# Optimization experiments

Hardware: AMD Instinct MI355X
Metric: run time of the kernel (lower is better)

## Reference

```python
import jax, jax.numpy as jnp
import numpy as np

TOP_K = 2

def setup_inputs() -> dict:
    key = jax.random.key(0)
    ks = jax.random.split(key, 8)
    B, T, C, E, I, S = 1, 2048, 2048, 8, 1408, 2816
    s = 0.02  # weight scale for numerical stability
    return {
        "x": jax.random.normal(ks[0], (B, T, C), jnp.float32),
        "gate_w": jax.random.normal(ks[1], (E, C), jnp.float32) * s,
        "w1": jax.random.normal(ks[2], (E, I, C), jnp.float32) * s,
        "w3": jax.random.normal(ks[3], (E, I, C), jnp.float32) * s,
        "w2": jax.random.normal(ks[4], (E, C, I), jnp.float32) * s,
        "sw1": jax.random.normal(ks[5], (S, C), jnp.float32) * s,
        "sw3": jax.random.normal(ks[6], (S, C), jnp.float32) * s,
        "sw2": jax.random.normal(ks[7], (C, S), jnp.float32) * s,
    }

def reference(x, gate_w, w1, w3, w2, sw1, sw3, sw2):
    B, T, C = x.shape
    E = gate_w.shape[0]
    xf = x.reshape(-1, C)                      # [N, C]
    N = xf.shape[0]
    # --- routing: top-k of raw logits, softmax over the k selected logits ---
    logits = xf @ gate_w.T                     # [N, E]
    pv, idx = jax.lax.top_k(logits, TOP_K)     # [N, K]
    pv = jax.nn.softmax(pv.astype(jnp.float32), axis=-1).astype(x.dtype)
    # token-expert combine weights (sum of probs per expert, scatter of top-k)
    tew = jnp.zeros((N, E), x.dtype).at[jnp.arange(N)[:, None], idx].add(pv)
    # --- experts (SwiGLU), computed densely over all experts and masked by tew ---
    h = jax.nn.silu(jnp.einsum('nc,eic->nei', xf, w1)) * jnp.einsum('nc,eic->nei', xf, w3)
    eo = jnp.einsum('nei,eci->nec', h, w2)     # [N, E, C]
    y = jnp.einsum('nec,ne->nc', eo, tew).reshape(B, T, C)
    # --- shared expert on the residual input ---
    sh = (jax.nn.silu(x @ sw1.T) * (x @ sw3.T)) @ sw2.T
    return y + sh
```

## Files before the change

### kernel.cpp

```cpp
#include <hip/hip_runtime.h>

#define DEVI __device__ __forceinline__

typedef __attribute__((ext_vector_type(4))) float f32x4;
typedef __attribute__((ext_vector_type(8))) short bf16x8;

static constexpr int NT = 2048;
static constexpr int CD = 2048;
static constexpr int NE = 8;
static constexpr int ID = 1408;
static constexpr int SD = 2816;
static constexpr int ROWS = 2 * NT;
static constexpr int ROWS_PAD = ROWS + 256;

DEVI unsigned short f2bf(float f) {
  unsigned u = __builtin_bit_cast(unsigned, f);
  u += 0x7fff + ((u >> 16) & 1);
  return (unsigned short)(u >> 16);
}
DEVI float bf2f(unsigned short s) { return __builtin_bit_cast(float, (unsigned)s << 16); }
DEVI float silu_f(float z) { return z / (1.f + __expf(-z)); }

DEVI void gll16(const void* g, void* l) {
  __builtin_amdgcn_global_load_lds((__attribute__((address_space(1))) void*)(void*)g,
                                   (__attribute__((address_space(3))) void*)l, 16, 0, 0);
}

DEVI void bar_sched() {
  __builtin_amdgcn_s_barrier();
  __builtin_amdgcn_sched_barrier(0);
}
DEVI void wait_vm8() { asm volatile("s_waitcnt vmcnt(8)" ::: "memory"); }
DEVI void wait_vm0() { asm volatile("s_waitcnt vmcnt(0)" ::: "memory"); }
DEVI void wait_lgk0() { asm volatile("s_waitcnt lgkmcnt(0)" ::: "memory"); }

DEVI int swz8(int bid, int nwg) {
  constexpr int CH = 8, G = 64;
  int nfull = nwg - (nwg % G);
  if (bid >= nfull) return bid;
  int c = bid / G, r = bid % G;
  return c * G + (r % 8) * CH + (r / 8);
}

__global__ __launch_bounds__(256) void k_cvt(const float* __restrict__ s,
                                             unsigned short* __restrict__ d, int n8)
{
  int i = blockIdx.x * 256 + threadIdx.x;
  int stride = gridDim.x * 256;
  for (; i < n8; i += stride) {
    float4 a = ((const float4*)s)[2 * i];
    float4 b = ((const float4*)s)[2 * i + 1];
    ushort4 p0 = make_ushort4(f2bf(a.x), f2bf(a.y), f2bf(a.z), f2bf(a.w));
    ushort4 p1 = make_ushort4(f2bf(b.x), f2bf(b.y), f2bf(b.z), f2bf(b.w));
    ((ushort4*)d)[2 * i]     = p0;
    ((ushort4*)d)[2 * i + 1] = p1;
  }
}

__global__ __launch_bounds__(64) void k_router(const float* __restrict__ x,
    const float* __restrict__ gw, int* __restrict__ counts,
    int* __restrict__ eidx, int* __restrict__ posn, float* __restrict__ probs)
{
  const int n = blockIdx.x;
  const int lane = threadIdx.x;
  const float4* xr = (const float4*)(x + (size_t)n * CD);
  float acc[NE];
#pragma unroll
  for (int e = 0; e < NE; ++e) acc[e] = 0.f;
  for (int i = lane; i < CD / 4; i += 64) {
    float4 xv = xr[i];
#pragma unroll
    for (int e = 0; e < NE; ++e) {
      float4 gv = ((const float4*)(gw + (size_t)e * CD))[i];
      acc[e] += xv.x * gv.x + xv.y * gv.y + xv.z * gv.z + xv.w * gv.w;
    }
  }
#pragma unroll
  for (int e = 0; e < NE; ++e) {
    float v = acc[e];
#pragma unroll
    for (int off = 32; off > 0; off >>= 1) v += __shfl_down(v, off);
    acc[e] = v;
  }
  if (lane == 0) {
    int b0 = 0; float m0 = acc[0];
#pragma unroll
    for (int e = 1; e < NE; ++e) if (acc[e] > m0) { m0 = acc[e]; b0 = e; }
    int b1 = -1; float m1 = 0.f;
#pragma unroll
    for (int e = 0; e < NE; ++e) {
      if (e == b0) continue;
      if (b1 < 0 || acc[e] > m1) { m1 = acc[e]; b1 = e; }
    }
    float d = __expf(m1 - m0);
    float inv = 1.f / (1.f + d);
    eidx[2 * n] = b0; eidx[2 * n + 1] = b1;
    probs[2 * n] = inv; probs[2 * n + 1] = d * inv;
    posn[2 * n] = atomicAdd(&counts[b0], 1);
    posn[2 * n + 1] = atomicAdd(&counts[b1], 1);
  }
}

__global__ void k_scan(const int* __restrict__ counts, int* __restrict__ bases) {
  if (threadIdx.x == 0) {
    int s = 0;
    for (int e = 0; e < NE; ++e) { bases[e] = s; s += counts[e]; }
  }
}

__global__ __launch_bounds__(256) void k_build(const int* __restrict__ eidx,
    const int* __restrict__ posn, const int* __restrict__ bases,
    int* __restrict__ rows_of, int* __restrict__ row2tok)
{
  int n = blockIdx.x * 256 + threadIdx.x;
  if (n >= NT) return;
#pragma unroll
  for (int k = 0; k < 2; ++k) {
    int e = eidx[2 * n + k];
    int row = bases[e] + posn[2 * n + k];
    rows_of[2 * n + k] = row;
    row2tok[row] = n;
  }
}

__global__ __launch_bounds__(512, 2) void k_up(
    const unsigned short* __restrict__ xb,
    const unsigned short* __restrict__ w1b, const unsigned short* __restrict__ w3b,
    const unsigned short* __restrict__ sw1b, const unsigned short* __restrict__ sw3b,
    unsigned short* __restrict__ h, unsigned short* __restrict__ hs,
    const int* __restrict__ counts, const int* __restrict__ bases,
    const int* __restrict__ row2tok)
{
  extern __shared__ char sm[];
  constexpr int NSH = (NT / 256) * (SD / 128);
  constexpr int NWG = NSH + NE * (ID / 128) * (NT / 256);
  constexpr int NSTEP = CD / 64;

  int lin = swz8((int)blockIdx.x, NWG);
  int cls, mx, pn, e = 0;
  if (lin < NSH) { cls = 0; mx = lin % 8; pn = lin / 8; }
  else { cls = 1; int r = lin - NSH; mx = r % 8; r /= 8; pn = r % 11; e = r / 11; }

  int M = NT, baserow = 0;
  if (cls) { M = counts[e]; if (mx * 256 >= M) return; baserow = bases[e]; }
  const int m0 = mx * 256, n0 = pn * 128;

  const unsigned short* B1 = cls ? w1b + ((size_t)e * ID + n0) * CD : sw1b + (size_t)n0 * CD;
  const unsigned short* B3 = cls ? w3b + ((size_t)e * ID + n0) * CD : sw3b + (size_t)n0 * CD;

  const int tid = threadIdx.x, l = tid & 63, w = tid >> 6;
  const int wr = w >> 2, wn = w & 3;
  const int slot = ((tid & 7) ^ ((tid >> 3) & 7)) * 16;

  const char* aP[4];
#pragma unroll
  for (int t = 0; t < 4; ++t) {
    int r = t * 64 + (tid >> 3);
    const unsigned short* rb;
    if (cls) {
      int grow = m0 + r; int gr = grow < M ? grow : 0;
      rb = xb + (size_t)row2tok[baserow + gr] * CD;
    } else {
      rb = xb + (size_t)(m0 + r) * CD;
    }
    aP[t] = (const char*)rb + slot;
  }
  const char* bP1[2]; const char* bP3[2];
#pragma unroll
  for (int t = 0; t < 2; ++t) {
    int r = t * 64 + (tid >> 3);
    bP1[t] = (const char*)(B1 + (size_t)r * CD) + slot;
    bP3[t] = (const char*)(B3 + (size_t)r * CD) + slot;
  }

  f32x4 acc1[8][2], acc3[8][2];
#pragma unroll
  for (int m = 0; m < 8; ++m)
#pragma unroll
    for (int n = 0; n < 2; ++n) {
      acc1[m][n] = {0.f, 0.f, 0.f, 0.f};
      acc3[m][n] = {0.f, 0.f, 0.f, 0.f};
    }

  const int lrow = l & 15, lkg = l >> 4, l7 = l & 7;
  const int ao0 = (lkg ^ l7) * 16, ao1 = ((4 + lkg) ^ l7) * 16;

  auto stageF = [&](char* base, size_t kb) {
    char* sA = base; char* sB1 = base + 32768; char* sB3 = base + 49152;
#pragma unroll
    for (int t = 0; t < 4; ++t) gll16(aP[t] + kb, sA + t * 8192 + tid * 16);
#pragma unroll
    for (int t = 0; t < 2; ++t) {
      gll16(bP1[t] + kb, sB1 + t * 8192 + tid * 16);
      gll16(bP3[t] + kb, sB3 + t * 8192 + tid * 16);
    }
  };
  auto computeF = [&](const char* base) {
    const char* sA = base; const char* sB1 = base + 32768; const char* sB3 = base + 49152;
#pragma unroll
    for (int kk = 0; kk < 2; ++kk) {
      const int ao = kk ? ao1 : ao0;
      bf16x8 af[8];
#pragma unroll
      for (int m = 0; m < 8; ++m)
        af[m] = *(const bf16x8*)(sA + (wr * 128 + m * 16 + lrow) * 128 + ao);
#pragma unroll
      for (int n = 0; n < 2; ++n) {
        bf16x8 b1 = *(const bf16x8*)(sB1 + (wn * 32 + n * 16 + lrow) * 128 + ao);
        bf16x8 b3 = *(const bf16x8*)(sB3 + (wn * 32 + n * 16 + lrow) * 128 + ao);
#pragma unroll
        for (int m = 0; m < 8; ++m) {
          acc1[m][n] = __builtin_amdgcn_mfma_f32_16x16x32_bf16(af[m], b1, acc1[m][n], 0, 0, 0);
          acc3[m][n] = __builtin_amdgcn_mfma_f32_16x16x32_bf16(af[m], b3, acc3[m][n], 0, 0, 0);
        }
      }
    }
  };

  char* s0 = sm; char* s1 = sm + 65536;
  stageF(s0, 0);
  int t = 0;
  for (; t < NSTEP - 2; t += 2) {
    stageF(s1, (size_t)(t + 1) * 128);
    wait_vm8(); bar_sched();
    computeF(s0);
    wait_lgk0(); bar_sched();
    stageF(s0, (size_t)(t + 2) * 128);
    wait_vm8(); bar_sched();
    computeF(s1);
    wait_lgk0(); bar_sched();
  }
  stageF(s1, (size_t)(NSTEP - 1) * 128);
  wait_vm8(); bar_sched();
  computeF(s0);
  wait_vm0(); bar_sched();
  computeF(s1);

#pragma unroll
  for (int m = 0; m < 8; ++m) {
    int rb_ = m0 + wr * 128 + m * 16 + lkg * 4;
#pragma unroll
    for (int j = 0; j < 4; ++j) {
      int grow = rb_ + j;
      if (cls && grow >= M) continue;
#pragma unroll
      for (int n = 0; n < 2; ++n) {
        int gcol = n0 + wn * 32 + n * 16 + lrow;
        float hh = silu_f(acc1[m][n][j]) * acc3[m][n][j];
        if (cls) h[(size_t)(baserow + grow) * ID + gcol] = f2bf(hh);
        else     hs[(size_t)grow * SD + gcol] = f2bf(hh);
      }
    }
  }
}

__global__ __launch_bounds__(512, 2) void k_down(
    const unsigned short* __restrict__ h, const unsigned short* __restrict__ hs,
    const unsigned short* __restrict__ w2b, const unsigned short* __restrict__ sw2b,
    unsigned short* __restrict__ eo, float* __restrict__ y,
    const int* __restrict__ counts, const int* __restrict__ bases)
{
  extern __shared__ char sm[];
  constexpr int NRT = NE * (CD / 256) * (NT / 256);
  constexpr int NWG = NRT + (CD / 256) * (NT / 256);

  int lin = swz8((int)blockIdx.x, NWG);
  int cls, mx, pn, e = 0;
  if (lin < NRT) { cls = 1; mx = lin % 8; int r = lin / 8; pn = r % 8; e = r / 8; }
  else { cls = 0; int r = lin - NRT; mx = r % 8; pn = r / 8; }

  int M = NT, baserow = 0;
  if (cls) { M = counts[e]; if (mx * 256 >= M) return; baserow = bases[e]; }
  const int m0 = mx * 256, n0 = pn * 256;
  const int KD_ = cls ? ID : SD;
  const int nstep = KD_ / 64;

  const unsigned short* B = cls ? w2b + ((size_t)e * CD + n0) * ID : sw2b + (size_t)n0 * SD;

  const int tid = threadIdx.x, l = tid & 63, w = tid >> 6;
  const int wr = w >> 2, wn = w & 3;
  const int slot = ((tid & 7) ^ ((tid >> 3) & 7)) * 16;

  const char* aP[4]; const char* bP[4];
#pragma unroll
  for (int t = 0; t < 4; ++t) {
    int r = t * 64 + (tid >> 3);
    const unsigned short* rb = cls ? h + (size_t)(baserow + m0 + r) * ID
                                   : hs + (size_t)(m0 + r) * SD;
    aP[t] = (const char*)rb + slot;
    bP[t] = (const char*)(B + (size_t)r * KD_) + slot;
  }

  f32x4 acc[8][4];
#pragma unroll
  for (int m = 0; m < 8; ++m)
#pragma unroll
    for (int n = 0; n < 4; ++n) acc[m][n] = {0.f, 0.f, 0.f, 0.f};

  const int lrow = l & 15, lkg = l >> 4, l7 = l & 7;
  const int ao0 = (lkg ^ l7) * 16, ao1 = ((4 + lkg) ^ l7) * 16;

  auto stageF = [&](char* base, size_t kb) {
    char* sA = base; char* sB = base + 32768;
#pragma unroll
    for (int t = 0; t < 4; ++t) {
      gll16(aP[t] + kb, sA + t * 8192 + tid * 16);
      gll16(bP[t] + kb, sB + t * 8192 + tid * 16);
    }
  };
  auto computeF = [&](const char* base) {
    const char* sA = base; const char* sB = base + 32768;
#pragma unroll
    for (int kk = 0; kk < 2; ++kk) {
      const int ao = kk ? ao1 : ao0;
      bf16x8 af[8];
#pragma unroll
      for (int m = 0; m < 8; ++m)
        af[m] = *(const bf16x8*)(sA + (wr * 128 + m * 16 + lrow) * 128 + ao);
#pragma unroll
      for (int n = 0; n < 4; ++n) {
        bf16x8 bv = *(const bf16x8*)(sB + (wn * 64 + n * 16 + lrow) * 128 + ao);
#pragma unroll
        for (int m = 0; m < 8; ++m)
          acc[m][n] = __builtin_amdgcn_mfma_f32_16x16x32_bf16(af[m], bv, acc[m][n], 0, 0, 0);
      }
    }
  };

  char* s0 = sm; char* s1 = sm + 65536;
  stageF(s0, 0);
  int t = 0;
  for (; t < nstep - 2; t += 2) {
    stageF(s1, (size_t)(t + 1) * 128);
    wait_vm8(); bar_sched();
    computeF(s0);
    wait_lgk0(); bar_sched();
    stageF(s0, (size_t)(t + 2) * 128);
    wait_vm8(); bar_sched();
    computeF(s1);
    wait_lgk0(); bar_sched();
  }
  stageF(s1, (size_t)(nstep - 1) * 128);
  wait_vm8(); bar_sched();
  computeF(s0);
  wait_vm0(); bar_sched();
  computeF(s1);

#pragma unroll
  for (int m = 0; m < 8; ++m) {
    int rb_ = m0 + wr * 128 + m * 16 + lkg * 4;
#pragma unroll
    for (int j = 0; j < 4; ++j) {
      int grow = rb_ + j;
      if (cls && grow >= M) continue;
#pragma unroll
      for (int n = 0; n < 4; ++n) {
        int gcol = n0 + wn * 64 + n * 16 + lrow;
        float v = acc[m][n][j];
        if (cls) eo[(size_t)(baserow + grow) * CD + gcol] = f2bf(v);
        else     y[(size_t)grow * CD + gcol] = v;
      }
    }
  }
}

__global__ __launch_bounds__(256) void k_combine(float* __restrict__ y,
    const unsigned short* __restrict__ eo, const int* __restrict__ rows_of,
    const float* __restrict__ probs)
{
  const int n = blockIdx.x;
  const int c = threadIdx.x * 8;
  const int r0 = rows_of[2 * n], r1 = rows_of[2 * n + 1];
  const float p0 = probs[2 * n], p1 = probs[2 * n + 1];
  bf16x8 e0 = *(const bf16x8*)(eo + (size_t)r0 * CD + c);
  bf16x8 e1 = *(const bf16x8*)(eo + (size_t)r1 * CD + c);
  float* yp = y + (size_t)n * CD + c;
  float4 y0 = *(float4*)yp, y1 = *(float4*)(yp + 4);
  y0.x += p0 * bf2f((unsigned short)e0[0]) + p1 * bf2f((unsigned short)e1[0]);
  y0.y += p0 * bf2f((unsigned short)e0[1]) + p1 * bf2f((unsigned short)e1[1]);
  y0.z += p0 * bf2f((unsigned short)e0[2]) + p1 * bf2f((unsigned short)e1[2]);
  y0.w += p0 * bf2f((unsigned short)e0[3]) + p1 * bf2f((unsigned short)e1[3]);
  y1.x += p0 * bf2f((unsigned short)e0[4]) + p1 * bf2f((unsigned short)e1[4]);
  y1.y += p0 * bf2f((unsigned short)e0[5]) + p1 * bf2f((unsigned short)e1[5]);
  y1.z += p0 * bf2f((unsigned short)e0[6]) + p1 * bf2f((unsigned short)e1[6]);
  y1.w += p0 * bf2f((unsigned short)e0[7]) + p1 * bf2f((unsigned short)e1[7]);
  *(float4*)yp = y0; *(float4*)(yp + 4) = y1;
}

extern "C" void kernel_launch(void* const* d_in, const int* in_sizes, int n_in,
                              void* d_out, int out_size, void* d_ws, size_t ws_size,
                              hipStream_t stream)
{
  const float* x   = (const float*)d_in[0];
  const float* gw  = (const float*)d_in[1];
  const float* w1  = (const float*)d_in[2];
  const float* w3  = (const float*)d_in[3];
  const float* w2  = (const float*)d_in[4];
  const float* sw1 = (const float*)d_in[5];
  const float* sw3 = (const float*)d_in[6];
  const float* sw2 = (const float*)d_in[7];
  float* y = (float*)d_out;

  char* p = (char*)d_ws;
  auto alloc = [&](size_t b) { char* r = p; p += (b + 255) & ~(size_t)255; return r; };
  int*   counts  = (int*)alloc(NE * 4);
  int*   bases   = (int*)alloc(NE * 4);
  int*   eidx    = (int*)alloc((size_t)NT * 2 * 4);
  int*   posn    = (int*)alloc((size_t)NT * 2 * 4);
  float* probs   = (float*)alloc((size_t)NT * 2 * 4);
  int*   rows_of = (int*)alloc((size_t)NT * 2 * 4);
  int*   row2tok = (int*)alloc((size_t)ROWS * 4);
  unsigned short* xb   = (unsigned short*)alloc((size_t)NT * CD * 2);
  unsigned short* w1b  = (unsigned short*)alloc((size_t)NE * ID * CD * 2);
  unsigned short* w3b  = (unsigned short*)alloc((size_t)NE * ID * CD * 2);
  unsigned short* w2b  = (unsigned short*)alloc((size_t)NE * CD * ID * 2);
  unsigned short* sw1b = (unsigned short*)alloc((size_t)SD * CD * 2);
  unsigned short* sw3b = (unsigned short*)alloc((size_t)SD * CD * 2);
  unsigned short* sw2b = (unsigned short*)alloc((size_t)CD * SD * 2);
  unsigned short* h    = (unsigned short*)alloc((size_t)ROWS_PAD * ID * 2);
  unsigned short* eo   = (unsigned short*)alloc((size_t)ROWS_PAD * CD * 2);
  unsigned short* hs   = (unsigned short*)alloc((size_t)NT * SD * 2);

  hipFuncSetAttribute((const void*)k_up,   hipFuncAttributeMaxDynamicSharedMemorySize, 131072);
  hipFuncSetAttribute((const void*)k_down, hipFuncAttributeMaxDynamicSharedMemorySize, 131072);

  hipMemsetAsync(counts, 0, NE * 4, stream);

  auto cvt = [&](const float* s, unsigned short* d, size_t n) {
    int n8 = (int)(n / 8);
    int grid = (n8 + 255) / 256; if (grid > 2048) grid = 2048;
    k_cvt<<<grid, 256, 0, stream>>>(s, d, n8);
  };
  cvt(x,   xb,   (size_t)NT * CD);
  cvt(w1,  w1b,  (size_t)NE * ID * CD);
  cvt(w3,  w3b,  (size_t)NE * ID * CD);
  cvt(w2,  w2b,  (size_t)NE * CD * ID);
  cvt(sw1, sw1b, (size_t)SD * CD);
  cvt(sw3, sw3b, (size_t)SD * CD);
  cvt(sw2, sw2b, (size_t)CD * SD);

  k_router<<<NT, 64, 0, stream>>>(x, gw, counts, eidx, posn, probs);
  k_scan<<<1, 64, 0, stream>>>(counts, bases);
  k_build<<<NT / 256, 256, 0, stream>>>(eidx, posn, bases, rows_of, row2tok);

  {
    constexpr int NWG = (NT / 256) * (SD / 128) + NE * (ID / 128) * (NT / 256);
    k_up<<<NWG, 512, 131072, stream>>>(xb, w1b, w3b, sw1b, sw3b, h, hs,
                                       counts, bases, row2tok);
  }
  {
    constexpr int NWG = NE * (CD / 256) * (NT / 256) + (CD / 256) * (NT / 256);
    k_down<<<NWG, 512, 131072, stream>>>(h, hs, w2b, sw2b, eo, y, counts, bases);
  }
  k_combine<<<NT, 256, 0, stream>>>(y, eo, rows_of, probs);
}
```

Measured before the change: 468.9 us.

## Restructure GEMM main loops into ping-pong register-fragment pipeline with split staging

Both GEMM kernels replace the stage-then-compute double-buffer loop with a finer schedule. The LDS-to-register fragment loads for each half of the M tile are interleaved with MFMA batches on the other half. The global-to-LDS loads for the next k-step are split into A and B halves and issued between compute chunks, and s_setprio raises wave priority around the MFMA blocks. The aim is to hide LDS read latency and global load issue behind matrix math, at the cost of one barrier with a full vmcnt(0) wait per k-step and more live fragment registers.

```diff
diff --git a/kernel.cpp b/kernel.cpp
--- a/kernel.cpp
+++ b/kernel.cpp
@@ -30,7 +30,7 @@
   __builtin_amdgcn_s_barrier();
   __builtin_amdgcn_sched_barrier(0);
 }
-DEVI void wait_vm8() { asm volatile("s_waitcnt vmcnt(8)" ::: "memory"); }
+DEVI void sched0() { __builtin_amdgcn_sched_barrier(0); }
 DEVI void wait_vm0() { asm volatile("s_waitcnt vmcnt(0)" ::: "memory"); }
 DEVI void wait_lgk0() { asm volatile("s_waitcnt lgkmcnt(0)" ::: "memory"); }
 
@@ -183,58 +183,71 @@
     }
 
   const int lrow = l & 15, lkg = l >> 4, l7 = l & 7;
-  const int ao0 = (lkg ^ l7) * 16, ao1 = ((4 + lkg) ^ l7) * 16;
-
-  auto stageF = [&](char* base, size_t kb) {
-    char* sA = base; char* sB1 = base + 32768; char* sB3 = base + 49152;
-#pragma unroll
-    for (int t = 0; t < 4; ++t) gll16(aP[t] + kb, sA + t * 8192 + tid * 16);
+
+  auto stage_first = [&](char* base, size_t kb) {
+#pragma unroll
+    for (int t = 0; t < 4; ++t) gll16(aP[t] + kb, base + t * 8192 + tid * 16);
+  };
+  auto stage_second = [&](char* base, size_t kb) {
+    char* sB1 = base + 32768; char* sB3 = base + 49152;
 #pragma unroll
     for (int t = 0; t < 2; ++t) {
       gll16(bP1[t] + kb, sB1 + t * 8192 + tid * 16);
       gll16(bP3[t] + kb, sB3 + t * 8192 + tid * 16);
     }
   };
-  auto computeF = [&](const char* base) {
-    const char* sA = base; const char* sB1 = base + 32768; const char* sB3 = base + 49152;
-#pragma unroll
-    for (int kk = 0; kk < 2; ++kk) {
-      const int ao = kk ? ao1 : ao0;
-      bf16x8 af[8];
-#pragma unroll
-      for (int m = 0; m < 8; ++m)
-        af[m] = *(const bf16x8*)(sA + (wr * 128 + m * 16 + lrow) * 128 + ao);
-#pragma unroll
-      for (int n = 0; n < 2; ++n) {
-        bf16x8 b1 = *(const bf16x8*)(sB1 + (wn * 32 + n * 16 + lrow) * 128 + ao);
-        bf16x8 b3 = *(const bf16x8*)(sB3 + (wn * 32 + n * 16 + lrow) * 128 + ao);
-#pragma unroll
-        for (int m = 0; m < 8; ++m) {
-          acc1[m][n] = __builtin_amdgcn_mfma_f32_16x16x32_bf16(af[m], b1, acc1[m][n], 0, 0, 0);
-          acc3[m][n] = __builtin_amdgcn_mfma_f32_16x16x32_bf16(af[m], b3, acc3[m][n], 0, 0, 0);
-        }
+  auto ldq = [&](bf16x8* fa, bf16x8* fb1, bf16x8* fb3, const char* cur, int mh, int kk) {
+    const char* sA = cur; const char* sB1 = cur + 32768; const char* sB3 = cur + 49152;
+    const int ao = ((kk * 4 + lkg) ^ l7) * 16;
+#pragma unroll
+    for (int m = 0; m < 4; ++m)
+      fa[m] = *(const bf16x8*)(sA + (wr * 128 + mh * 64 + m * 16 + lrow) * 128 + ao);
+#pragma unroll
+    for (int n = 0; n < 2; ++n) {
+      fb1[n] = *(const bf16x8*)(sB1 + (wn * 32 + n * 16 + lrow) * 128 + ao);
+      fb3[n] = *(const bf16x8*)(sB3 + (wn * 32 + n * 16 + lrow) * 128 + ao);
+    }
+  };
+  auto mmq = [&](const bf16x8* fa, const bf16x8* fb1, const bf16x8* fb3, int mh) {
+    __builtin_amdgcn_s_setprio(1);
+#pragma unroll
+    for (int n = 0; n < 2; ++n)
+#pragma unroll
+      for (int m = 0; m < 4; ++m) {
+        acc1[mh * 4 + m][n] = __builtin_amdgcn_mfma_f32_16x16x32_bf16(fa[m], fb1[n], acc1[mh * 4 + m][n], 0, 0, 0);
+        acc3[mh * 4 + m][n] = __builtin_amdgcn_mfma_f32_16x16x32_bf16(fa[m], fb3[n], acc3[mh * 4 + m][n], 0, 0, 0);
       }
-    }
-  };
-
-  char* s0 = sm; char* s1 = sm + 65536;
-  stageF(s0, 0);
-  int t = 0;
-  for (; t < NSTEP - 2; t += 2) {
-    stageF(s1, (size_t)(t + 1) * 128);
-    wait_vm8(); bar_sched();
-    computeF(s0);
-    wait_lgk0(); bar_sched();
-    stageF(s0, (size_t)(t + 2) * 128);
-    wait_vm8(); bar_sched();
-    computeF(s1);
-    wait_lgk0(); bar_sched();
-  }
-  stageF(s1, (size_t)(NSTEP - 1) * 128);
-  wait_vm8(); bar_sched();
-  computeF(s0);
+    __builtin_amdgcn_s_setprio(0);
+  };
+
+  stage_first(sm, 0);
+  stage_second(sm, 0);
   wait_vm0(); bar_sched();
-  computeF(s1);
+
+  bf16x8 Xa[4], Xb1[2], Xb3[2], Ya[4], Yb1[2], Yb3[2];
+
+  for (int t = 0; t < NSTEP; ++t) {
+    char* cur = sm + (size_t)(t & 1) * 65536;
+    char* nxt = sm + (size_t)((t + 1) & 1) * 65536;
+    size_t kb = (size_t)(t + 1) * 128;
+    ldq(Xa, Xb1, Xb3, cur, 0, 0);
+    sched0();
+    if (t + 1 < NSTEP) stage_first(nxt, kb);
+    ldq(Ya, Yb1, Yb3, cur, 1, 0);
+    mmq(Xa, Xb1, Xb3, 0);
+    sched0();
+    if (t + 1 < NSTEP) stage_second(nxt, kb);
+    ldq(Xa, Xb1, Xb3, cur, 0, 1);
+    mmq(Ya, Yb1, Yb3, 1);
+    sched0();
+    ldq(Ya, Yb1, Yb3, cur, 1, 1);
+    mmq(Xa, Xb1, Xb3, 0);
+    sched0();
+    mmq(Ya, Yb1, Yb3, 1);
+    sched0();
+    wait_vm0(); wait_lgk0();
+    bar_sched();
+  }
 
 #pragma unroll
   for (int m = 0; m < 8; ++m) {
@@ -298,53 +311,64 @@
     for (int n = 0; n < 4; ++n) acc[m][n] = {0.f, 0.f, 0.f, 0.f};
 
   const int lrow = l & 15, lkg = l >> 4, l7 = l & 7;
-  const int ao0 = (lkg ^ l7) * 16, ao1 = ((4 + lkg) ^ l7) * 16;
-
-  auto stageF = [&](char* base, size_t kb) {
-    char* sA = base; char* sB = base + 32768;
-#pragma unroll
-    for (int t = 0; t < 4; ++t) {
-      gll16(aP[t] + kb, sA + t * 8192 + tid * 16);
-      gll16(bP[t] + kb, sB + t * 8192 + tid * 16);
-    }
-  };
-  auto computeF = [&](const char* base) {
-    const char* sA = base; const char* sB = base + 32768;
-#pragma unroll
-    for (int kk = 0; kk < 2; ++kk) {
-      const int ao = kk ? ao1 : ao0;
-      bf16x8 af[8];
-#pragma unroll
-      for (int m = 0; m < 8; ++m)
-        af[m] = *(const bf16x8*)(sA + (wr * 128 + m * 16 + lrow) * 128 + ao);
-#pragma unroll
-      for (int n = 0; n < 4; ++n) {
-        bf16x8 bv = *(const bf16x8*)(sB + (wn * 64 + n * 16 + lrow) * 128 + ao);
-#pragma unroll
-        for (int m = 0; m < 8; ++m)
-          acc[m][n] = __builtin_amdgcn_mfma_f32_16x16x32_bf16(af[m], bv, acc[m][n], 0, 0, 0);
-      }
-    }
-  };
-
-  char* s0 = sm; char* s1 = sm + 65536;
-  stageF(s0, 0);
-  int t = 0;
-  for (; t < nstep - 2; t += 2) {
-    stageF(s1, (size_t)(t + 1) * 128);
-    wait_vm8(); bar_sched();
-    computeF(s0);
-    wait_lgk0(); bar_sched();
-    stageF(s0, (size_t)(t + 2) * 128);
-    wait_vm8(); bar_sched();
-    computeF(s1);
-    wait_lgk0(); bar_sched();
-  }
-  stageF(s1, (size_t)(nstep - 1) * 128);
-  wait_vm8(); bar_sched();
-  computeF(s0);
+
+  auto stage_first = [&](char* base, size_t kb) {
+#pragma unroll
+    for (int t = 0; t < 4; ++t) gll16(aP[t] + kb, base + t * 8192 + tid * 16);
+  };
+  auto stage_second = [&](char* base, size_t kb) {
+    char* sB = base + 32768;
+#pragma unroll
+    for (int t = 0; t < 4; ++t) gll16(bP[t] + kb, sB + t * 8192 + tid * 16);
+  };
+  auto ldq = [&](bf16x8* fa, bf16x8* fb, const char* cur, int mh, int kk) {
+    const char* sA = cur; const char* sB = cur + 32768;
+    const int ao = ((kk * 4 + lkg) ^ l7) * 16;
+#pragma unroll
+    for (int m = 0; m < 4; ++m)
+      fa[m] = *(const bf16x8*)(sA + (wr * 128 + mh * 64 + m * 16 + lrow) * 128 + ao);
+#pragma unroll
+    for (int n = 0; n < 4; ++n)
+      fb[n] = *(const bf16x8*)(sB + (wn * 64 + n * 16 + lrow) * 128 + ao);
+  };
+  auto mmq = [&](const bf16x8* fa, const bf16x8* fb, int mh) {
+    __builtin_amdgcn_s_setprio(1);
+#pragma unroll
+    for (int n = 0; n < 4; ++n)
+#pragma unroll
+      for (int m = 0; m < 4; ++m)
+        acc[mh * 4 + m][n] = __builtin_amdgcn_mfma_f32_16x16x32_bf16(fa[m], fb[n], acc[mh * 4 + m][n], 0, 0, 0);
+    __builtin_amdgcn_s_setprio(0);
+  };
+
+  stage_first(sm, 0);
+  stage_second(sm, 0);
   wait_vm0(); bar_sched();
-  computeF(s1);
+
+  bf16x8 Xa[4], Xb[4], Ya[4], Yb[4];
+
+  for (int t = 0; t < nstep; ++t) {
+    char* cur = sm + (size_t)(t & 1) * 65536;
+    char* nxt = sm + (size_t)((t + 1) & 1) * 65536;
+    size_t kb = (size_t)(t + 1) * 128;
+    ldq(Xa, Xb, cur, 0, 0);
+    sched0();
+    if (t + 1 < nstep) stage_first(nxt, kb);
+    ldq(Ya, Yb, cur, 1, 0);
+    mmq(Xa, Xb, 0);
+    sched0();
+    if (t + 1 < nstep) stage_second(nxt, kb);
+    ldq(Xa, Xb, cur, 0, 1);
+    mmq(Ya, Yb, 1);
+    sched0();
+    ldq(Ya, Yb, cur, 1, 1);
+    mmq(Xa, Xb, 0);
+    sched0();
+    mmq(Ya, Yb, 1);
+    sched0();
+    wait_vm0(); wait_lgk0();
+    bar_sched();
+  }
 
 #pragma unroll
   for (int m = 0; m < 8; ++m) {
```

Result: faster. 437.1 us (-6.8%).
